# Performance work log

Measured on AMD Instinct MI355X. Metric: run time of the kernel, lower is better.

The kernel has to match this reference:

```python
import jax, jax.numpy as jnp
import numpy as np

N_NODES = 100000
THETA = jnp.asarray([0.2, -0.4, 0.3, -0.15, 0.05], dtype=jnp.float32)


def setup_inputs() -> dict:
    key = jax.random.key(0)
    k1, k2, k3, k4 = jax.random.split(key, 4)
    n_edges = 1600000
    feat = jax.random.normal(k1, (N_NODES, 32), dtype=jnp.float32)
    src = jax.random.randint(k2, (n_edges,), 0, N_NODES, dtype=jnp.int32)
    dst = jax.random.randint(k3, (n_edges,), 0, N_NODES, dtype=jnp.int32)
    mask = jax.random.uniform(k4, (n_edges,), dtype=jnp.float32)
    return {"feat": feat, "src": src, "dst": dst, "mask": mask}


def reference(feat, src, dst, mask):
    # degree = sum of edge mask into destination nodes (copy_e + sum)
    deg = jax.ops.segment_sum(mask, dst, num_segments=N_NODES)
    # D^{-1/2} with clamp(min=1)
    d_invsqrt = jnp.power(jnp.maximum(deg, 1.0), -0.5)[:, None]  # [N,1]

    h = THETA[0] * feat
    for k in range(1, THETA.shape[0]):
        # unnormalized Laplacian step: feat - D^{-1/2} A D^{-1/2} feat
        scaled = feat * d_invsqrt                      # [N,d]
        msg = scaled[src] * mask[:, None]              # [E,d] gather + edge scale
        agg = jax.ops.segment_sum(msg, dst, num_segments=N_NODES)  # [N,d]
        feat = feat - agg * d_invsqrt
        h = h + THETA[k] * feat
    return h
```

## Files before the change

kernel.cpp:

```cpp
#include <hip/hip_runtime.h>
#include <hip/hip_fp16.h>


#define FDIM 32
#define DLO_BITS 8
#define BKT_NODES 256
#define NBLK 512
#define MAXBKT 512


__global__ __launch_bounds__(256) void p1_kernel(const int* __restrict__ dst,
                                                 int* __restrict__ cntT,
                                                 int nbkt, int S, int E) {
    __shared__ int lh[MAXBKT];
    int b = blockIdx.x;
    for (int t = threadIdx.x; t < MAXBKT; t += 256) lh[t] = 0;
    __syncthreads();
    int e0 = b * S;
    int e1 = e0 + S < E ? e0 + S : E;
    for (int e = e0 + threadIdx.x; e < e1; e += 256)
        atomicAdd(&lh[dst[e] >> DLO_BITS], 1);
    __syncthreads();
    for (int t = threadIdx.x; t < nbkt; t += 256) cntT[t * NBLK + b] = lh[t];
}

__global__ void scanA_kernel(const int* __restrict__ cntT, int* __restrict__ obase,
                             int* __restrict__ bsums, int M2) {
    int tid = threadIdx.x;
    int gid = blockIdx.x * 256 + tid;
    int v = (gid < M2) ? cntT[gid] : 0;
    int lane = tid & 63, wv = tid >> 6;
    int x = v;
#pragma unroll
    for (int o = 1; o < 64; o <<= 1) {
        int y = __shfl_up(x, o);
        if (lane >= o) x += y;
    }
    __shared__ int ws[4];
    if (lane == 63) ws[wv] = x;
    __syncthreads();
    int add = 0;
    for (int i = 0; i < wv; ++i) add += ws[i];
    x += add;
    if (gid < M2) obase[gid] = x - v;
    if (tid == 255) bsums[blockIdx.x] = x;
}

__global__ void scan2_kernel(int* __restrict__ bsums, int nb) {
    __shared__ int ws[8];
    __shared__ int carry;
    if (threadIdx.x == 0) carry = 0;
    __syncthreads();
    for (int base = 0; base < nb; base += 512) {
        int i = base + threadIdx.x;
        int v = (i < nb) ? bsums[i] : 0;
        int lane = threadIdx.x & 63, wv = threadIdx.x >> 6;
        int x = v;
#pragma unroll
        for (int o = 1; o < 64; o <<= 1) {
            int y = __shfl_up(x, o);
            if (lane >= o) x += y;
        }
        if (lane == 63) ws[wv] = x;
        __syncthreads();
        int add = 0;
        for (int j = 0; j < wv; ++j) add += ws[j];
        x += add;
        int c = carry;
        if (i < nb) bsums[i] = x - v + c;
        __syncthreads();
        if (threadIdx.x == 511) carry = c + x;
        __syncthreads();
    }
}

__global__ void scanC_kernel(int* __restrict__ obase, const int* __restrict__ bsums, int M2) {
    int gid = blockIdx.x * 256 + threadIdx.x;
    if (gid < M2) obase[gid] += bsums[blockIdx.x];
}

__global__ __launch_bounds__(256) void p3_kernel(const int* __restrict__ src,
                                                 const int* __restrict__ dst,
                                                 const float* __restrict__ mask,
                                                 const int* __restrict__ obase,
                                                 int2* __restrict__ esp,
                                                 int S, int E) {
    __shared__ int lh[MAXBKT];
    int b = blockIdx.x;
    for (int t = threadIdx.x; t < MAXBKT; t += 256) lh[t] = 0;
    __syncthreads();
    int e0 = b * S;
    int e1 = e0 + S < E ? e0 + S : E;
    for (int e = e0 + threadIdx.x; e < e1; e += 256) {
        int d = dst[e];
        int g = d >> DLO_BITS;
        int r = atomicAdd(&lh[g], 1);
        int pos = obase[g * NBLK + b] + r;
        int2 v;
        v.x = src[e] | ((d & (BKT_NODES - 1)) << 17);
        v.y = __float_as_int(mask[e]);
        esp[pos] = v;
    }
}

__global__ __launch_bounds__(256) void p4_kernel(const int2* __restrict__ esp,
                                                 const int* __restrict__ obase,
                                                 int* __restrict__ esI,
                                                 int* __restrict__ row_ptr,
                                                 float* __restrict__ dinv,
                                                 const float4* __restrict__ feat,
                                                 uint2* __restrict__ m0,
                                                 int nbkt, int N, int E) {
    __shared__ int lcnt[BKT_NODES];
    __shared__ int lofs[BKT_NODES];
    __shared__ float ldeg[BKT_NODES];
    __shared__ int ws[4];
    int g = blockIdx.x;
    int tid = threadIdx.x;
    lcnt[tid] = 0;
    ldeg[tid] = 0.0f;
    __syncthreads();
    int segbase = obase[g * NBLK];
    int segend = (g + 1 < nbkt) ? obase[(g + 1) * NBLK] : E;
    for (int i = segbase + tid; i < segend; i += 256) {
        int2 v = esp[i];
        int dlo = v.x >> 17;
        atomicAdd(&lcnt[dlo], 1);
        atomicAdd(&ldeg[dlo], __int_as_float(v.y));
    }
    __syncthreads();
    int v = lcnt[tid];
    int lane = tid & 63, wv = tid >> 6;
    int x = v;
#pragma unroll
    for (int o = 1; o < 64; o <<= 1) {
        int y = __shfl_up(x, o);
        if (lane >= o) x += y;
    }
    if (lane == 63) ws[wv] = x;
    __syncthreads();
    int add = 0;
    for (int i = 0; i < wv; ++i) add += ws[i];
    x += add;
    int excl = x - v;
    lofs[tid] = excl;
    int node = g * BKT_NODES + tid;
    if (node < N) {
        row_ptr[node] = segbase + excl;
        float d = ldeg[tid];
        d = d > 1.0f ? d : 1.0f;
        float di = 1.0f / sqrtf(d);
        dinv[node] = di;
        ldeg[tid] = di;
    }
    if (g == 0 && tid == 0) row_ptr[N] = E;
    __syncthreads();
    lcnt[tid] = 0;
    __syncthreads();
    for (int i = segbase + tid; i < segend; i += 256) {
        int2 v2 = esp[i];
        int dlo = v2.x >> 17;
        int r = atomicAdd(&lcnt[dlo], 1);
        float mk = __int_as_float(v2.y);
        int wq = (int)(mk * 32768.0f + 0.5f);
        if (wq > 32767) wq = 32767;
        esI[segbase + lofs[dlo] + r] = (v2.x & 0x1FFFF) | (wq << 17);
    }
    int base_node = g * BKT_NODES;
    for (int t = tid; t < BKT_NODES * 8; t += 256) {
        int nl = t >> 3;
        int n2 = base_node + nl;
        if (n2 >= N) break;
        float di = ldeg[nl];
        float4 f = feat[(size_t)n2 * 8 + (t & 7)];
        __half2 a = __float22half2_rn(make_float2(f.x * di, f.y * di));
        __half2 b = __float22half2_rn(make_float2(f.z * di, f.w * di));
        uint2 m;
        m.x = *(unsigned*)&a;
        m.y = *(unsigned*)&b;
        m0[(size_t)n2 * 8 + (t & 7)] = m;
    }
}

template <int MODE>
__global__ __launch_bounds__(256) void aggregate_kernel(
    const float4* __restrict__ fown, float4* __restrict__ fwr,
    const uint2* __restrict__ gin, uint2* __restrict__ gout,
    float4* __restrict__ out,
    const int* __restrict__ row_ptr, const int* __restrict__ es,
    const float* __restrict__ dinv, float theta, float theta0, int N) {
    int wave = (blockIdx.x * blockDim.x + threadIdx.x) >> 6;
    int lane = threadIdx.x & 63;
    int node = wave * 2 + (lane >> 5);
    if (node >= N) return;
    int lane32 = lane & 31;
    int c = lane32 & 7;
    int q = lane32 >> 3;
    int b = row_ptr[node];
    int e = row_ptr[node + 1];
    float ax = 0.f, ay = 0.f, az = 0.f, aw = 0.f;
    float bx = 0.f, by = 0.f, bz = 0.f, bw = 0.f;
    int i = b + q;
    for (; i + 4 < e; i += 8) {
        int e0 = es[i];
        int e1 = es[i + 4];
        float w0 = (float)((unsigned)e0 >> 17) * (1.0f / 32768.0f);
        float w1 = (float)((unsigned)e1 >> 17) * (1.0f / 32768.0f);
        uint2 r0 = gin[(size_t)(e0 & 0x1FFFF) * 8 + c];
        uint2 r1 = gin[(size_t)(e1 & 0x1FFFF) * 8 + c];
        float2 p0 = __half22float2(*(const __half2*)&r0.x);
        float2 p1 = __half22float2(*(const __half2*)&r0.y);
        float2 p2 = __half22float2(*(const __half2*)&r1.x);
        float2 p3 = __half22float2(*(const __half2*)&r1.y);
        ax += w0 * p0.x; ay += w0 * p0.y; az += w0 * p1.x; aw += w0 * p1.y;
        bx += w1 * p2.x; by += w1 * p2.y; bz += w1 * p3.x; bw += w1 * p3.y;
    }
    if (i < e) {
        int e0 = es[i];
        float w0 = (float)((unsigned)e0 >> 17) * (1.0f / 32768.0f);
        uint2 r0 = gin[(size_t)(e0 & 0x1FFFF) * 8 + c];
        float2 p0 = __half22float2(*(const __half2*)&r0.x);
        float2 p1 = __half22float2(*(const __half2*)&r0.y);
        ax += w0 * p0.x; ay += w0 * p0.y; az += w0 * p1.x; aw += w0 * p1.y;
    }
    ax += bx; ay += by; az += bz; aw += bw;
#pragma unroll
    for (int o = 8; o < 32; o <<= 1) {
        ax += __shfl_xor(ax, o);
        ay += __shfl_xor(ay, o);
        az += __shfl_xor(az, o);
        aw += __shfl_xor(aw, o);
    }
    if (q >= 3) return;
    float4 fav = fown[(size_t)node * 8 + c];
    float di = dinv[node];
    float fx = fav.x - ax * di;
    float fy = fav.y - ay * di;
    float fz = fav.z - az * di;
    float fw = fav.w - aw * di;
    if (MODE != 2) {
        if (q == 0) {
            float4 t; t.x = fx; t.y = fy; t.z = fz; t.w = fw;
            fwr[(size_t)node * 8 + c] = t;
        } else if (q == 1) {
            float4 o;
            if (MODE == 1) {
                o.x = theta0 * fav.x + theta * fx;
                o.y = theta0 * fav.y + theta * fy;
                o.z = theta0 * fav.z + theta * fz;
                o.w = theta0 * fav.w + theta * fw;
            } else {
                o = out[(size_t)node * 8 + c];
                o.x += theta * fx; o.y += theta * fy;
                o.z += theta * fz; o.w += theta * fw;
            }
            out[(size_t)node * 8 + c] = o;
        } else {
            __half2 a = __float22half2_rn(make_float2(fx * di, fy * di));
            __half2 bb = __float22half2_rn(make_float2(fz * di, fw * di));
            uint2 m;
            m.x = *(unsigned*)&a;
            m.y = *(unsigned*)&bb;
            gout[(size_t)node * 8 + c] = m;
        }
    } else {
        if (q == 1) {
            float4 o = out[(size_t)node * 8 + c];
            o.x += theta * fx; o.y += theta * fy;
            o.z += theta * fz; o.w += theta * fw;
            out[(size_t)node * 8 + c] = o;
        }
    }
}


__global__ void fb_deg_kernel(const int* __restrict__ dst, const float* __restrict__ mask,
                              float* __restrict__ deg, int E) {
    int e = blockIdx.x * blockDim.x + threadIdx.x;
    if (e < E) atomicAdd(&deg[dst[e]], mask[e]);
}

__global__ void fb_dinv_kernel(float* __restrict__ deg, int N) {
    int i = blockIdx.x * blockDim.x + threadIdx.x;
    if (i < N) {
        float d = deg[i];
        d = d > 1.0f ? d : 1.0f;
        deg[i] = 1.0f / sqrtf(d);
    }
}

__global__ void fb_init_kernel(const float4* __restrict__ feat, float4* __restrict__ fbuf,
                               float4* __restrict__ out, int n4) {
    int i = blockIdx.x * blockDim.x + threadIdx.x;
    if (i < n4) {
        float4 f = feat[i];
        fbuf[i] = f;
        float4 o;
        o.x = 0.2f * f.x; o.y = 0.2f * f.y; o.z = 0.2f * f.z; o.w = 0.2f * f.w;
        out[i] = o;
    }
}

__global__ void fb_scatter_kernel(const float4* __restrict__ fbuf, const float* __restrict__ dinv,
                                  const int* __restrict__ src, const int* __restrict__ dst,
                                  const float* __restrict__ mask, float* __restrict__ agg, int E) {
    int t = blockIdx.x * blockDim.x + threadIdx.x;
    int e = t >> 3;
    if (e >= E) return;
    int c4 = t & 7;
    int s = src[e];
    int d = dst[e];
    float w = mask[e] * dinv[s];
    float4 f = fbuf[s * 8 + c4];
    float* ap = agg + (size_t)d * FDIM + c4 * 4;
    atomicAdd(ap + 0, f.x * w);
    atomicAdd(ap + 1, f.y * w);
    atomicAdd(ap + 2, f.z * w);
    atomicAdd(ap + 3, f.w * w);
}

__global__ void fb_update_kernel(float4* __restrict__ fbuf, float4* __restrict__ agg,
                                 const float* __restrict__ dinv, float4* __restrict__ out,
                                 float theta, int n4) {
    int t = blockIdx.x * blockDim.x + threadIdx.x;
    if (t >= n4) return;
    int node = t >> 3;
    float di = dinv[node];
    float4 a = agg[t];
    float4 z; z.x = 0.f; z.y = 0.f; z.z = 0.f; z.w = 0.f;
    agg[t] = z;
    float4 f = fbuf[t];
    f.x -= a.x * di; f.y -= a.y * di; f.z -= a.z * di; f.w -= a.w * di;
    fbuf[t] = f;
    float4 o = out[t];
    o.x += theta * f.x; o.y += theta * f.y; o.z += theta * f.z; o.w += theta * f.w;
    out[t] = o;
}


static inline size_t align_up(size_t x) { return (x + 63) & ~(size_t)63; }

extern "C" void kernel_launch(void* const* d_in, const int* in_sizes, int n_in,
                              void* d_out, int out_size, void* d_ws, size_t ws_size,
                              hipStream_t stream) {
    const float* feat = (const float*)d_in[0];
    const int* src = (const int*)d_in[1];
    const int* dst = (const int*)d_in[2];
    const float* mask = (const float*)d_in[3];
    float* out = (float*)d_out;

    const int N = in_sizes[0] / FDIM;
    const int E = in_sizes[1];
    const float thetas[5] = {0.2f, -0.4f, 0.3f, -0.15f, 0.05f};
    const int B = 256;

    const int nbkt = (N + BKT_NODES - 1) / BKT_NODES;
    const int M2 = nbkt * NBLK;
    const int S = (E + NBLK - 1) / NBLK;
    const int nbM2 = (M2 + B - 1) / B;

    size_t o_dinv = 0;
    size_t o_rp   = align_up(o_dinv + N);
    size_t o_esI  = align_up(o_rp + N + 1);
    size_t o_m0   = align_up(o_esI + (size_t)E);
    size_t o_m1   = align_up(o_m0 + (size_t)N * 16);
    size_t o_big  = align_up(o_m1 + (size_t)N * 16);
    size_t o_esp  = o_big;
    size_t o_cntT = align_up(o_esp + 2 * (size_t)E);
    size_t o_ob   = align_up(o_cntT + (size_t)M2);
    size_t o_bs   = align_up(o_ob + (size_t)M2);
    size_t build_end = o_bs + 4096;
    size_t o_f    = o_big;
    size_t agg_end = o_f + (size_t)N * FDIM;
    size_t need = (build_end > agg_end ? build_end : agg_end) * 4;

    float* wsf = (float*)d_ws;
    int* wsi = (int*)d_ws;

    int nbE = (E + B - 1) / B;
    int nbN = (N + B - 1) / B;

    if (ws_size >= need && N <= (1 << 17) && nbkt <= MAXBKT) {
        float* dinv = wsf + o_dinv;
        int* row_ptr = wsi + o_rp;
        int* esI = wsi + o_esI;
        uint2* m0 = (uint2*)(wsi + o_m0);
        uint2* m1 = (uint2*)(wsi + o_m1);
        int2* esp = (int2*)(wsi + o_esp);
        int* cntT = wsi + o_cntT;
        int* obase = wsi + o_ob;
        int* bsums = wsi + o_bs;
        float4* f = (float4*)(wsf + o_f);

        p1_kernel<<<NBLK, B, 0, stream>>>(dst, cntT, nbkt, S, E);
        scanA_kernel<<<nbM2, B, 0, stream>>>(cntT, obase, bsums, M2);
        scan2_kernel<<<1, 512, 0, stream>>>(bsums, nbM2);
        scanC_kernel<<<nbM2, B, 0, stream>>>(obase, bsums, M2);
        p3_kernel<<<NBLK, B, 0, stream>>>(src, dst, mask, obase, esp, S, E);
        p4_kernel<<<nbkt, B, 0, stream>>>(esp, obase, esI, row_ptr, dinv,
                                          (const float4*)feat, m0, nbkt, N, E);

        int aggWaves = (N + 1) / 2;
        int agg_blocks = (aggWaves * 64 + B - 1) / B;
        aggregate_kernel<1><<<agg_blocks, B, 0, stream>>>((const float4*)feat, f, m0, m1,
                                                          (float4*)out, row_ptr, esI, dinv,
                                                          thetas[1], thetas[0], N);
        aggregate_kernel<0><<<agg_blocks, B, 0, stream>>>(f, f, m1, m0, (float4*)out,
                                                          row_ptr, esI, dinv, thetas[2], 0.f, N);
        aggregate_kernel<0><<<agg_blocks, B, 0, stream>>>(f, f, m0, m1, (float4*)out,
                                                          row_ptr, esI, dinv, thetas[3], 0.f, N);
        aggregate_kernel<2><<<agg_blocks, B, 0, stream>>>(f, f, m1, m0, (float4*)out,
                                                          row_ptr, esI, dinv, thetas[4], 0.f, N);
    } else {
        float* deg = wsf;
        float* agg = deg + align_up(N);
        float* fbuf = agg + (size_t)N * FDIM;

        hipMemsetAsync(d_ws, 0, (align_up(N) + (size_t)N * FDIM) * 4, stream);
        fb_deg_kernel<<<nbE, B, 0, stream>>>(dst, mask, deg, E);
        fb_dinv_kernel<<<nbN, B, 0, stream>>>(deg, N);

        int n4 = N * (FDIM / 4);
        fb_init_kernel<<<(n4 + B - 1) / B, B, 0, stream>>>((const float4*)feat, (float4*)fbuf,
                                                           (float4*)out, n4);
        long long sc_threads = (long long)E * 8;
        int sc_blocks = (int)((sc_threads + B - 1) / B);
        for (int k = 1; k < 5; ++k) {
            fb_scatter_kernel<<<sc_blocks, B, 0, stream>>>((const float4*)fbuf, deg, src, dst,
                                                           mask, agg, E);
            fb_update_kernel<<<(n4 + B - 1) / B, B, 0, stream>>>((float4*)fbuf, (float4*)agg,
                                                                 deg, (float4*)out, thetas[k], n4);
        }
    }
}
```

Baseline: 195.4 us.

## Pack four nodes per wave in aggregation, widen p4 blocks, double histogram blocks

The aggregate kernel now gives each node 16 lanes instead of 32 (4 nodes per wave). The cross-lane reduction shrinks to a single shuffle, and the q==0 lanes now write both the fp32 feature and the fp16 scaled message. p4 runs with 512 threads per bucket and the edge-partition block count doubles to 1024, with a guard on the scan size. The aim is better lane utilisation and more parallelism in the CSR build, at the cost of fewer edges in flight per node and more scan work.

```diff
diff --git a/kernel.cpp b/kernel.cpp
--- a/kernel.cpp
+++ b/kernel.cpp
@@ -5,7 +5,7 @@
 #define FDIM 32
 #define DLO_BITS 8
 #define BKT_NODES 256
-#define NBLK 512
+#define NBLK 1024
 #define MAXBKT 512
 
 
@@ -103,7 +103,7 @@
     }
 }
 
-__global__ __launch_bounds__(256) void p4_kernel(const int2* __restrict__ esp,
+__global__ __launch_bounds__(512) void p4_kernel(const int2* __restrict__ esp,
                                                  const int* __restrict__ obase,
                                                  int* __restrict__ esI,
                                                  int* __restrict__ row_ptr,
@@ -114,22 +114,21 @@
     __shared__ int lcnt[BKT_NODES];
     __shared__ int lofs[BKT_NODES];
     __shared__ float ldeg[BKT_NODES];
-    __shared__ int ws[4];
+    __shared__ int ws[8];
     int g = blockIdx.x;
     int tid = threadIdx.x;
-    lcnt[tid] = 0;
-    ldeg[tid] = 0.0f;
+    if (tid < BKT_NODES) { lcnt[tid] = 0; ldeg[tid] = 0.0f; }
     __syncthreads();
     int segbase = obase[g * NBLK];
     int segend = (g + 1 < nbkt) ? obase[(g + 1) * NBLK] : E;
-    for (int i = segbase + tid; i < segend; i += 256) {
+    for (int i = segbase + tid; i < segend; i += 512) {
         int2 v = esp[i];
         int dlo = v.x >> 17;
         atomicAdd(&lcnt[dlo], 1);
         atomicAdd(&ldeg[dlo], __int_as_float(v.y));
     }
     __syncthreads();
-    int v = lcnt[tid];
+    int v = (tid < BKT_NODES) ? lcnt[tid] : 0;
     int lane = tid & 63, wv = tid >> 6;
     int x = v;
 #pragma unroll
@@ -143,21 +142,23 @@
     for (int i = 0; i < wv; ++i) add += ws[i];
     x += add;
     int excl = x - v;
-    lofs[tid] = excl;
-    int node = g * BKT_NODES + tid;
-    if (node < N) {
-        row_ptr[node] = segbase + excl;
-        float d = ldeg[tid];
-        d = d > 1.0f ? d : 1.0f;
-        float di = 1.0f / sqrtf(d);
-        dinv[node] = di;
-        ldeg[tid] = di;
+    if (tid < BKT_NODES) {
+        lofs[tid] = excl;
+        int node = g * BKT_NODES + tid;
+        if (node < N) {
+            row_ptr[node] = segbase + excl;
+            float d = ldeg[tid];
+            d = d > 1.0f ? d : 1.0f;
+            float di = 1.0f / sqrtf(d);
+            dinv[node] = di;
+            ldeg[tid] = di;
+        }
     }
     if (g == 0 && tid == 0) row_ptr[N] = E;
     __syncthreads();
-    lcnt[tid] = 0;
-    __syncthreads();
-    for (int i = segbase + tid; i < segend; i += 256) {
+    if (tid < BKT_NODES) lcnt[tid] = 0;
+    __syncthreads();
+    for (int i = segbase + tid; i < segend; i += 512) {
         int2 v2 = esp[i];
         int dlo = v2.x >> 17;
         int r = atomicAdd(&lcnt[dlo], 1);
@@ -167,7 +168,7 @@
         esI[segbase + lofs[dlo] + r] = (v2.x & 0x1FFFF) | (wq << 17);
     }
     int base_node = g * BKT_NODES;
-    for (int t = tid; t < BKT_NODES * 8; t += 256) {
+    for (int t = tid; t < BKT_NODES * 8; t += 512) {
         int nl = t >> 3;
         int n2 = base_node + nl;
         if (n2 >= N) break;
@@ -191,19 +192,19 @@
     const float* __restrict__ dinv, float theta, float theta0, int N) {
     int wave = (blockIdx.x * blockDim.x + threadIdx.x) >> 6;
     int lane = threadIdx.x & 63;
-    int node = wave * 2 + (lane >> 5);
+    int node = wave * 4 + (lane >> 4);
     if (node >= N) return;
-    int lane32 = lane & 31;
-    int c = lane32 & 7;
-    int q = lane32 >> 3;
+    int l16 = lane & 15;
+    int c = l16 & 7;
+    int q = l16 >> 3;
     int b = row_ptr[node];
     int e = row_ptr[node + 1];
     float ax = 0.f, ay = 0.f, az = 0.f, aw = 0.f;
     float bx = 0.f, by = 0.f, bz = 0.f, bw = 0.f;
     int i = b + q;
-    for (; i + 4 < e; i += 8) {
+    for (; i + 2 < e; i += 4) {
         int e0 = es[i];
-        int e1 = es[i + 4];
+        int e1 = es[i + 2];
         float w0 = (float)((unsigned)e0 >> 17) * (1.0f / 32768.0f);
         float w1 = (float)((unsigned)e1 >> 17) * (1.0f / 32768.0f);
         uint2 r0 = gin[(size_t)(e0 & 0x1FFFF) * 8 + c];
@@ -224,14 +225,10 @@
         ax += w0 * p0.x; ay += w0 * p0.y; az += w0 * p1.x; aw += w0 * p1.y;
     }
     ax += bx; ay += by; az += bz; aw += bw;
-#pragma unroll
-    for (int o = 8; o < 32; o <<= 1) {
-        ax += __shfl_xor(ax, o);
-        ay += __shfl_xor(ay, o);
-        az += __shfl_xor(az, o);
-        aw += __shfl_xor(aw, o);
-    }
-    if (q >= 3) return;
+    ax += __shfl_xor(ax, 8);
+    ay += __shfl_xor(ay, 8);
+    az += __shfl_xor(az, 8);
+    aw += __shfl_xor(aw, 8);
     float4 fav = fown[(size_t)node * 8 + c];
     float di = dinv[node];
     float fx = fav.x - ax * di;
@@ -242,7 +239,13 @@
         if (q == 0) {
             float4 t; t.x = fx; t.y = fy; t.z = fz; t.w = fw;
             fwr[(size_t)node * 8 + c] = t;
-        } else if (q == 1) {
+            __half2 a = __float22half2_rn(make_float2(fx * di, fy * di));
+            __half2 bb = __float22half2_rn(make_float2(fz * di, fw * di));
+            uint2 m;
+            m.x = *(unsigned*)&a;
+            m.y = *(unsigned*)&bb;
+            gout[(size_t)node * 8 + c] = m;
+        } else {
             float4 o;
             if (MODE == 1) {
                 o.x = theta0 * fav.x + theta * fx;
@@ -255,13 +258,6 @@
                 o.z += theta * fz; o.w += theta * fw;
             }
             out[(size_t)node * 8 + c] = o;
-        } else {
-            __half2 a = __float22half2_rn(make_float2(fx * di, fy * di));
-            __half2 bb = __float22half2_rn(make_float2(fz * di, fw * di));
-            uint2 m;
-            m.x = *(unsigned*)&a;
-            m.y = *(unsigned*)&bb;
-            gout[(size_t)node * 8 + c] = m;
         }
     } else {
         if (q == 1) {
@@ -380,7 +376,7 @@
     int nbE = (E + B - 1) / B;
     int nbN = (N + B - 1) / B;
 
-    if (ws_size >= need && N <= (1 << 17) && nbkt <= MAXBKT) {
+    if (ws_size >= need && N <= (1 << 17) && nbkt <= MAXBKT && nbM2 <= 4096) {
         float* dinv = wsf + o_dinv;
         int* row_ptr = wsi + o_rp;
         int* esI = wsi + o_esI;
@@ -397,10 +393,10 @@
         scan2_kernel<<<1, 512, 0, stream>>>(bsums, nbM2);
         scanC_kernel<<<nbM2, B, 0, stream>>>(obase, bsums, M2);
         p3_kernel<<<NBLK, B, 0, stream>>>(src, dst, mask, obase, esp, S, E);
-        p4_kernel<<<nbkt, B, 0, stream>>>(esp, obase, esI, row_ptr, dinv,
-                                          (const float4*)feat, m0, nbkt, N, E);
-
-        int aggWaves = (N + 1) / 2;
+        p4_kernel<<<nbkt, 512, 0, stream>>>(esp, obase, esI, row_ptr, dinv,
+                                            (const float4*)feat, m0, nbkt, N, E);
+
+        int aggWaves = (N + 3) / 4;
         int agg_blocks = (aggWaves * 64 + B - 1) / B;
         aggregate_kernel<1><<<agg_blocks, B, 0, stream>>>((const float4*)feat, f, m0, m1,
                                                           (float4*)out, row_ptr, esI, dinv,
```

New measurement: 194.3 us. Within noise of the previous version (-0.6%).
